# Optimization experiments

Hardware: AMD Instinct MI355X
Metric: run time of the kernel (lower is better)

Reference implementation:

```python
import jax, jax.numpy as jnp
import numpy as np

R = 32          # voxel resolution
EPS = 0.0       # normalization eps


def setup_inputs() -> dict:
    key = jax.random.key(0)
    k1, k2 = jax.random.split(key)
    B, D, N = 16, 64, 32768
    features = jax.random.normal(k1, (B, D, N), dtype=jnp.float32)
    coords = jax.random.normal(k2, (B, 3, N), dtype=jnp.float32)
    return {"features": features, "coords": coords}


def reference(features, coords):
    """features: (B, D, N), coords: (B, 3, N).
    Returns (voxel_features (B, D, R, R, R), norm_coords (B, 3, N))."""
    B, D, N = features.shape
    r = R

    # --- normalize coords into [0, r-1] (torch detaches coords; fwd math identical) ---
    nc = coords - coords.mean(axis=2, keepdims=True)                    # center
    norm = jnp.linalg.norm(nc, axis=1, keepdims=True)                   # (B,1,N)
    max_norm = norm.max(axis=2, keepdims=True)                          # (B,1,1)
    nc = nc / (max_norm * 2.0 + EPS) + 0.5
    norm_coords = jnp.clip(nc * r, 0, r - 1)                            # (B,3,N)
    vox = jnp.round(norm_coords).astype(jnp.int32)                      # (B,3,N)

    # --- scatter-mean features into r^3 voxels (avg_voxelize) ---
    idx = vox[:, 0] * (r * r) + vox[:, 1] * r + vox[:, 2]               # (B,N) in [0, r^3)
    flat_idx = (idx + jnp.arange(B, dtype=jnp.int32)[:, None] * (r ** 3)).reshape(-1)  # (B*N,)
    flat_feat = features.transpose(0, 2, 1).reshape(B * N, D)           # (B*N, D)

    sums = jax.ops.segment_sum(flat_feat, flat_idx, num_segments=B * r ** 3)   # (B*r^3, D)
    cnt = jax.ops.segment_sum(jnp.ones((B * N,), dtype=features.dtype),
                              flat_idx, num_segments=B * r ** 3)               # (B*r^3,)
    avg = sums / jnp.maximum(cnt, 1.0)[:, None]                          # empty voxels -> 0

    vox_feat = avg.reshape(B, r ** 3, D).transpose(0, 2, 1).reshape(B, D, r, r, r)
    return vox_feat, norm_coords
```

## Files before the change

kernel.cpp:

```cpp
#include <hip/hip_runtime.h>

#define RES 32
#define R3 (RES * RES * RES)

__global__ __launch_bounds__(1024) void stats_kernel(
        const float* __restrict__ coords,
        float* __restrict__ mean_out,
        float* __restrict__ denom_out,
        int* __restrict__ counts, int N) {
    const int b = blockIdx.x;
    const int tid = threadIdx.x;
    const float* cb = coords + (size_t)b * 3 * N;

    int4* cz = (int4*)(counts + (size_t)b * R3);
    const int4 zi = make_int4(0, 0, 0, 0);
    for (int i = tid; i < (R3 >> 2); i += 1024) cz[i] = zi;

    const int nvec = N >> 2;
    const float4* c0 = (const float4*)cb;
    const float4* c1 = (const float4*)(cb + N);
    const float4* c2 = (const float4*)(cb + 2 * N);
    float s0 = 0.f, s1 = 0.f, s2 = 0.f;
    for (int n = tid; n < nvec; n += 1024) {
        float4 a = c0[n]; s0 += (a.x + a.y) + (a.z + a.w);
        float4 c = c1[n]; s1 += (c.x + c.y) + (c.z + c.w);
        float4 d = c2[n]; s2 += (d.x + d.y) + (d.z + d.w);
    }
    if (tid == 0) {
        for (int n = nvec << 2; n < N; ++n) {
            s0 += cb[n]; s1 += cb[N + n]; s2 += cb[2 * N + n];
        }
    }
    for (int off = 32; off; off >>= 1) {
        s0 += __shfl_down(s0, off);
        s1 += __shfl_down(s1, off);
        s2 += __shfl_down(s2, off);
    }
    __shared__ float r0[16], r1[16], r2[16];
    __shared__ float mean_s[3];
    const int lane = tid & 63, wv = tid >> 6;
    if (lane == 0) { r0[wv] = s0; r1[wv] = s1; r2[wv] = s2; }
    __syncthreads();
    if (tid == 0) {
        float t0 = 0.f, t1 = 0.f, t2 = 0.f;
        for (int w = 0; w < 16; ++w) { t0 += r0[w]; t1 += r1[w]; t2 += r2[w]; }
        mean_s[0] = t0 / (float)N;
        mean_s[1] = t1 / (float)N;
        mean_s[2] = t2 / (float)N;
    }
    __syncthreads();
    const float m0 = mean_s[0], m1 = mean_s[1], m2 = mean_s[2];

    float mx = 0.f;
    for (int n = tid; n < nvec; n += 1024) {
        float4 a = c0[n], c = c1[n], d = c2[n];
        a.x -= m0; a.y -= m0; a.z -= m0; a.w -= m0;
        c.x -= m1; c.y -= m1; c.z -= m1; c.w -= m1;
        d.x -= m2; d.y -= m2; d.z -= m2; d.w -= m2;
        mx = fmaxf(mx, a.x * a.x + c.x * c.x + d.x * d.x);
        mx = fmaxf(mx, a.y * a.y + c.y * c.y + d.y * d.y);
        mx = fmaxf(mx, a.z * a.z + c.z * c.z + d.z * d.z);
        mx = fmaxf(mx, a.w * a.w + c.w * c.w + d.w * d.w);
    }
    if (tid == 0) {
        for (int n = nvec << 2; n < N; ++n) {
            float a = cb[n] - m0, c = cb[N + n] - m1, d = cb[2 * N + n] - m2;
            mx = fmaxf(mx, a * a + c * c + d * d);
        }
    }
    for (int off = 32; off; off >>= 1) mx = fmaxf(mx, __shfl_down(mx, off));
    if (lane == 0) r0[wv] = mx;
    __syncthreads();
    if (tid == 0) {
        for (int w = 0; w < 16; ++w) mx = fmaxf(mx, r0[w]);
        mean_out[b * 4 + 0] = m0;
        mean_out[b * 4 + 1] = m1;
        mean_out[b * 4 + 2] = m2;
        denom_out[b] = 2.0f * sqrtf(mx);
    }
}

__global__ void point_kernel(const float* __restrict__ coords,
                             const float* __restrict__ mean,
                             const float* __restrict__ denom_in,
                             float* __restrict__ nc_out,
                             unsigned short* __restrict__ idx_out,
                             int* __restrict__ counts, int N) {
    const int n4 = blockIdx.x * blockDim.x + threadIdx.x;
    const int b = blockIdx.y;
    const int nvec = (N + 3) >> 2;
    if (n4 >= nvec) return;

    const float* cb = coords + (size_t)b * 3 * N;
    const float m0 = mean[b * 4 + 0];
    const float m1 = mean[b * 4 + 1];
    const float m2 = mean[b * 4 + 2];
    const float denom = denom_in[b];
    float* ncb = nc_out + (size_t)b * 3 * N;
    unsigned short* irow = idx_out + (size_t)b * N;
    int* crow = counts + (size_t)b * R3;

    const int n0 = n4 << 2;
    if (n0 + 3 < N) {
        float4 a = *(const float4*)(cb + n0);
        float4 c = *(const float4*)(cb + N + n0);
        float4 d = *(const float4*)(cb + 2 * N + n0);
        float4 v0, v1, v2;
        int4 id;
        #define PROC(comp)                                                        \
        {                                                                         \
            float x = (a.comp - m0) / denom + 0.5f;                               \
            float y = (c.comp - m1) / denom + 0.5f;                               \
            float z = (d.comp - m2) / denom + 0.5f;                               \
            v0.comp = fminf(fmaxf(x * (float)RES, 0.f), (float)(RES - 1));        \
            v1.comp = fminf(fmaxf(y * (float)RES, 0.f), (float)(RES - 1));        \
            v2.comp = fminf(fmaxf(z * (float)RES, 0.f), (float)(RES - 1));        \
            id.comp = (int)rintf(v0.comp) * RES * RES                             \
                    + (int)rintf(v1.comp) * RES + (int)rintf(v2.comp);            \
        }
        PROC(x) PROC(y) PROC(z) PROC(w)
        #undef PROC
        *(float4*)(ncb + n0) = v0;
        *(float4*)(ncb + N + n0) = v1;
        *(float4*)(ncb + 2 * N + n0) = v2;
        ushort4 us;
        us.x = (unsigned short)id.x; us.y = (unsigned short)id.y;
        us.z = (unsigned short)id.z; us.w = (unsigned short)id.w;
        *(ushort4*)(irow + n0) = us;
        atomicAdd(&crow[id.x], 1);
        atomicAdd(&crow[id.y], 1);
        atomicAdd(&crow[id.z], 1);
        atomicAdd(&crow[id.w], 1);
    } else {
        for (int n = n0; n < N; ++n) {
            float x = (cb[n] - m0) / denom + 0.5f;
            float y = (cb[N + n] - m1) / denom + 0.5f;
            float z = (cb[2 * N + n] - m2) / denom + 0.5f;
            float v0 = fminf(fmaxf(x * (float)RES, 0.f), (float)(RES - 1));
            float v1 = fminf(fmaxf(y * (float)RES, 0.f), (float)(RES - 1));
            float v2 = fminf(fmaxf(z * (float)RES, 0.f), (float)(RES - 1));
            ncb[n] = v0; ncb[N + n] = v1; ncb[2 * N + n] = v2;
            int id = (int)rintf(v0) * RES * RES + (int)rintf(v1) * RES + (int)rintf(v2);
            irow[n] = (unsigned short)id;
            atomicAdd(&crow[id], 1);
        }
    }
}

__global__ __launch_bounds__(1024) void scanplist_kernel(
        const int* __restrict__ counts,
        const unsigned short* __restrict__ idx,
        unsigned short* __restrict__ start,
        unsigned short* __restrict__ plist, int N) {
    const int b = blockIdx.x;
    const int tid = threadIdx.x;
    const int lane = tid & 63, wv = tid >> 6;
    const int base = tid * 32;
    const int* crow = counts + (size_t)b * R3;

    __shared__ int cursor[R3];
    __shared__ int wsum[16], woff[16];

    int vals[32];
    int tot = 0;
    const int4* c4 = (const int4*)(crow + base);
    for (int i = 0; i < 8; ++i) {
        int4 t = c4[i];
        vals[4 * i + 0] = t.x; vals[4 * i + 1] = t.y;
        vals[4 * i + 2] = t.z; vals[4 * i + 3] = t.w;
        tot += (t.x + t.y) + (t.z + t.w);
    }
    int inc = tot;
    for (int o = 1; o < 64; o <<= 1) {
        int t = __shfl_up(inc, o);
        if (lane >= o) inc += t;
    }
    if (lane == 63) wsum[wv] = inc;
    __syncthreads();
    if (tid == 0) {
        int r = 0;
        for (int w = 0; w < 16; ++w) { woff[w] = r; r += wsum[w]; }
    }
    __syncthreads();
    int run = woff[wv] + inc - tot;
    unsigned short* srow = start + (size_t)b * R3 + base;
    for (int i = 0; i < 32; ++i) {
        srow[i] = (unsigned short)run;
        cursor[base + i] = run;
        run += vals[i];
    }
    __syncthreads();

    const unsigned short* irow = idx + (size_t)b * N;
    unsigned short* prow = plist + (size_t)b * N;
    for (int n = tid; n < N; n += 1024) {
        const int v = irow[n];
        const int pos = atomicAdd(&cursor[v], 1);
        prow[pos] = (unsigned short)n;
    }
}

__global__ __launch_bounds__(1024) void reduce_kernel(
        const float* __restrict__ feats,
        const unsigned short* __restrict__ plist,
        const unsigned short* __restrict__ start,
        const int* __restrict__ counts,
        float* __restrict__ vox, int D, int N) {
    const int d = blockIdx.x;
    const int b = blockIdx.y;
    const int tid = threadIdx.x;

    __shared__ float row[R3];
    const float* frow = feats + ((size_t)b * D + d) * N;
    {
        float4* r4 = (float4*)row;
        const float4* f4 = (const float4*)frow;
        for (int i = tid; i < (N >> 2); i += 1024) r4[i] = f4[i];
        if (tid == 0) for (int n = (N >> 2) << 2; n < N; ++n) row[n] = frow[n];
    }
    __syncthreads();

    const unsigned short* prow = plist + (size_t)b * N;
    const unsigned short* srow = start + (size_t)b * R3;
    const int* crow = counts + (size_t)b * R3;
    float* vrow = vox + ((size_t)b * D + d) * R3;

    for (int k = 0; k < R3 / 1024; ++k) {
        const int v = (k << 10) + tid;
        const int c = crow[v];
        const int s = srow[v];
        float a = 0.f;
        int j = 0;
        for (; j + 16 <= c; j += 16) {
            const unsigned short* pp = prow + s + j;
            const int p0 = pp[0],  p1 = pp[1],  p2 = pp[2],  p3 = pp[3];
            const int p4 = pp[4],  p5 = pp[5],  p6 = pp[6],  p7 = pp[7];
            const int p8 = pp[8],  p9 = pp[9],  pa = pp[10], pb = pp[11];
            const int pc = pp[12], pd = pp[13], pe = pp[14], pf = pp[15];
            float t0 = ((row[p0] + row[p1]) + (row[p2] + row[p3]))
                     + ((row[p4] + row[p5]) + (row[p6] + row[p7]));
            float t1 = ((row[p8] + row[p9]) + (row[pa] + row[pb]))
                     + ((row[pc] + row[pd]) + (row[pe] + row[pf]));
            a += t0 + t1;
        }
        for (; j + 4 <= c; j += 4) {
            const unsigned short* pp = prow + s + j;
            const int p0 = pp[0], p1 = pp[1], p2 = pp[2], p3 = pp[3];
            a += (row[p0] + row[p1]) + (row[p2] + row[p3]);
        }
        for (; j < c; ++j) a += row[prow[s + j]];
        vrow[v] = a / (float)(c > 1 ? c : 1);
    }
}

extern "C" void kernel_launch(void* const* d_in, const int* in_sizes, int n_in,
                              void* d_out, int out_size, void* d_ws, size_t ws_size,
                              hipStream_t stream) {
    const float* feats  = (const float*)d_in[0];
    const float* coords = (const float*)d_in[1];
    float* out = (float*)d_out;

    const int D = (int)(3LL * in_sizes[0] / in_sizes[1]);
    const int B = (int)((long long)(out_size - in_sizes[1]) / ((long long)D * R3));
    const int N = in_sizes[1] / (3 * B);

    float* vox_out = out;
    float* nc_out  = out + (size_t)B * D * R3;

    const size_t BR3 = (size_t)B * R3;
    const size_t BN  = (size_t)B * N;
    float*          mean   = (float*)d_ws;
    float*          denom  = (float*)((char*)d_ws + 1024);
    int*            counts = (int*)((char*)d_ws + 4096);
    unsigned short* start  = (unsigned short*)((char*)d_ws + 4096 + 4 * BR3);
    unsigned short* idx    = (unsigned short*)((char*)d_ws + 4096 + 6 * BR3);
    unsigned short* plist  = (unsigned short*)((char*)d_ws + 4096 + 6 * BR3 + 2 * BN);

    stats_kernel<<<dim3(B), dim3(1024), 0, stream>>>(coords, mean, denom, counts, N);

    const int nvec = (N + 3) >> 2;
    point_kernel<<<dim3((nvec + 255) / 256, B), dim3(256), 0, stream>>>(
        coords, mean, denom, nc_out, idx, counts, N);

    scanplist_kernel<<<dim3(B), dim3(1024), 0, stream>>>(counts, idx, start, plist, N);

    reduce_kernel<<<dim3(D, B), dim3(1024), 0, stream>>>(
        feats, plist, start, counts, vox_out, D, N);
}
```

Baseline: 458.2 us.

## Fuse all voxelization stages into one cooperative persistent kernel with sorted-key segmented reduction

```diff
diff --git a/kernel.cpp b/kernel.cpp
--- a/kernel.cpp
+++ b/kernel.cpp
@@ -1,255 +1,297 @@
 #include <hip/hip_runtime.h>
-
-#define RES 32
-#define R3 (RES * RES * RES)
-
-__global__ __launch_bounds__(1024) void stats_kernel(
-        const float* __restrict__ coords,
-        float* __restrict__ mean_out,
-        float* __restrict__ denom_out,
-        int* __restrict__ counts, int N) {
-    const int b = blockIdx.x;
+#include <hip/hip_cooperative_groups.h>
+namespace cg = cooperative_groups;
+
+#define RES  32
+#define R3   32768
+#define NBLK 256
+#define NTHR 1024
+
+struct Params {
+    const float* feats;
+    const float* coords;
+    float* vox;
+    float* nc;
+    float* accum;
+    unsigned* maxsq;
+    int* counts;
+    unsigned short* start;
+    int* cursor;
+    unsigned* keys;
+    unsigned* skeys;
+    int B, D, N;
+};
+
+__global__ __launch_bounds__(NTHR, 4) void fused_kernel(Params p) {
+    cg::grid_group grid = cg::this_grid();
     const int tid = threadIdx.x;
-    const float* cb = coords + (size_t)b * 3 * N;
-
-    int4* cz = (int4*)(counts + (size_t)b * R3);
-    const int4 zi = make_int4(0, 0, 0, 0);
-    for (int i = tid; i < (R3 >> 2); i += 1024) cz[i] = zi;
-
+    const int bid = blockIdx.x;
+    const int B = p.B, D = p.D, N = p.N;
+    const int lane = tid & 63, wv = tid >> 6;
+
+    __shared__ float row[R3];
+    __shared__ float red[3][16];
+    __shared__ unsigned short headv[NTHR];
+    __shared__ float headsum[NTHR];
+    __shared__ unsigned char contf[NTHR];
+    __shared__ int wsum[16], woff[16];
+
+    {
+        const int gtid = bid * NTHR + tid, gsz = NBLK * NTHR;
+        int4* c4 = (int4*)p.counts;
+        const int tot4 = (B * R3) >> 2;
+        for (int i = gtid; i < tot4; i += gsz) c4[i] = make_int4(0, 0, 0, 0);
+        if (bid == 0) {
+            if (tid < B * 4) p.accum[tid] = 0.f;
+            if (tid >= 256 && tid < 256 + B) p.maxsq[tid - 256] = 0u;
+        }
+    }
+    grid.sync();
+
+    const int b1 = bid % B;
+    const int chunk = bid / B;
+    const int pstride = (NBLK / B) * NTHR;
+    const float* cb = p.coords + (size_t)b1 * 3 * N;
     const int nvec = N >> 2;
     const float4* c0 = (const float4*)cb;
     const float4* c1 = (const float4*)(cb + N);
     const float4* c2 = (const float4*)(cb + 2 * N);
-    float s0 = 0.f, s1 = 0.f, s2 = 0.f;
-    for (int n = tid; n < nvec; n += 1024) {
-        float4 a = c0[n]; s0 += (a.x + a.y) + (a.z + a.w);
-        float4 c = c1[n]; s1 += (c.x + c.y) + (c.z + c.w);
-        float4 d = c2[n]; s2 += (d.x + d.y) + (d.z + d.w);
-    }
-    if (tid == 0) {
-        for (int n = nvec << 2; n < N; ++n) {
-            s0 += cb[n]; s1 += cb[N + n]; s2 += cb[2 * N + n];
-        }
-    }
-    for (int off = 32; off; off >>= 1) {
-        s0 += __shfl_down(s0, off);
-        s1 += __shfl_down(s1, off);
-        s2 += __shfl_down(s2, off);
-    }
-    __shared__ float r0[16], r1[16], r2[16];
-    __shared__ float mean_s[3];
-    const int lane = tid & 63, wv = tid >> 6;
-    if (lane == 0) { r0[wv] = s0; r1[wv] = s1; r2[wv] = s2; }
-    __syncthreads();
-    if (tid == 0) {
-        float t0 = 0.f, t1 = 0.f, t2 = 0.f;
-        for (int w = 0; w < 16; ++w) { t0 += r0[w]; t1 += r1[w]; t2 += r2[w]; }
-        mean_s[0] = t0 / (float)N;
-        mean_s[1] = t1 / (float)N;
-        mean_s[2] = t2 / (float)N;
-    }
-    __syncthreads();
-    const float m0 = mean_s[0], m1 = mean_s[1], m2 = mean_s[2];
-
-    float mx = 0.f;
-    for (int n = tid; n < nvec; n += 1024) {
-        float4 a = c0[n], c = c1[n], d = c2[n];
-        a.x -= m0; a.y -= m0; a.z -= m0; a.w -= m0;
-        c.x -= m1; c.y -= m1; c.z -= m1; c.w -= m1;
-        d.x -= m2; d.y -= m2; d.z -= m2; d.w -= m2;
-        mx = fmaxf(mx, a.x * a.x + c.x * c.x + d.x * d.x);
-        mx = fmaxf(mx, a.y * a.y + c.y * c.y + d.y * d.y);
-        mx = fmaxf(mx, a.z * a.z + c.z * c.z + d.z * d.z);
-        mx = fmaxf(mx, a.w * a.w + c.w * c.w + d.w * d.w);
-    }
-    if (tid == 0) {
-        for (int n = nvec << 2; n < N; ++n) {
-            float a = cb[n] - m0, c = cb[N + n] - m1, d = cb[2 * N + n] - m2;
-            mx = fmaxf(mx, a * a + c * c + d * d);
-        }
-    }
-    for (int off = 32; off; off >>= 1) mx = fmaxf(mx, __shfl_down(mx, off));
-    if (lane == 0) r0[wv] = mx;
-    __syncthreads();
-    if (tid == 0) {
-        for (int w = 0; w < 16; ++w) mx = fmaxf(mx, r0[w]);
-        mean_out[b * 4 + 0] = m0;
-        mean_out[b * 4 + 1] = m1;
-        mean_out[b * 4 + 2] = m2;
-        denom_out[b] = 2.0f * sqrtf(mx);
-    }
-}
-
-__global__ void point_kernel(const float* __restrict__ coords,
-                             const float* __restrict__ mean,
-                             const float* __restrict__ denom_in,
-                             float* __restrict__ nc_out,
-                             unsigned short* __restrict__ idx_out,
-                             int* __restrict__ counts, int N) {
-    const int n4 = blockIdx.x * blockDim.x + threadIdx.x;
-    const int b = blockIdx.y;
-    const int nvec = (N + 3) >> 2;
-    if (n4 >= nvec) return;
-
-    const float* cb = coords + (size_t)b * 3 * N;
-    const float m0 = mean[b * 4 + 0];
-    const float m1 = mean[b * 4 + 1];
-    const float m2 = mean[b * 4 + 2];
-    const float denom = denom_in[b];
-    float* ncb = nc_out + (size_t)b * 3 * N;
-    unsigned short* irow = idx_out + (size_t)b * N;
-    int* crow = counts + (size_t)b * R3;
-
-    const int n0 = n4 << 2;
-    if (n0 + 3 < N) {
-        float4 a = *(const float4*)(cb + n0);
-        float4 c = *(const float4*)(cb + N + n0);
-        float4 d = *(const float4*)(cb + 2 * N + n0);
-        float4 v0, v1, v2;
-        int4 id;
-        #define PROC(comp)                                                        \
-        {                                                                         \
-            float x = (a.comp - m0) / denom + 0.5f;                               \
-            float y = (c.comp - m1) / denom + 0.5f;                               \
-            float z = (d.comp - m2) / denom + 0.5f;                               \
-            v0.comp = fminf(fmaxf(x * (float)RES, 0.f), (float)(RES - 1));        \
-            v1.comp = fminf(fmaxf(y * (float)RES, 0.f), (float)(RES - 1));        \
-            v2.comp = fminf(fmaxf(z * (float)RES, 0.f), (float)(RES - 1));        \
-            id.comp = (int)rintf(v0.comp) * RES * RES                             \
-                    + (int)rintf(v1.comp) * RES + (int)rintf(v2.comp);            \
-        }
-        PROC(x) PROC(y) PROC(z) PROC(w)
-        #undef PROC
-        *(float4*)(ncb + n0) = v0;
-        *(float4*)(ncb + N + n0) = v1;
-        *(float4*)(ncb + 2 * N + n0) = v2;
-        ushort4 us;
-        us.x = (unsigned short)id.x; us.y = (unsigned short)id.y;
-        us.z = (unsigned short)id.z; us.w = (unsigned short)id.w;
-        *(ushort4*)(irow + n0) = us;
-        atomicAdd(&crow[id.x], 1);
-        atomicAdd(&crow[id.y], 1);
-        atomicAdd(&crow[id.z], 1);
-        atomicAdd(&crow[id.w], 1);
-    } else {
-        for (int n = n0; n < N; ++n) {
-            float x = (cb[n] - m0) / denom + 0.5f;
-            float y = (cb[N + n] - m1) / denom + 0.5f;
-            float z = (cb[2 * N + n] - m2) / denom + 0.5f;
-            float v0 = fminf(fmaxf(x * (float)RES, 0.f), (float)(RES - 1));
-            float v1 = fminf(fmaxf(y * (float)RES, 0.f), (float)(RES - 1));
-            float v2 = fminf(fmaxf(z * (float)RES, 0.f), (float)(RES - 1));
-            ncb[n] = v0; ncb[N + n] = v1; ncb[2 * N + n] = v2;
-            int id = (int)rintf(v0) * RES * RES + (int)rintf(v1) * RES + (int)rintf(v2);
-            irow[n] = (unsigned short)id;
-            atomicAdd(&crow[id], 1);
-        }
-    }
-}
-
-__global__ __launch_bounds__(1024) void scanplist_kernel(
-        const int* __restrict__ counts,
-        const unsigned short* __restrict__ idx,
-        unsigned short* __restrict__ start,
-        unsigned short* __restrict__ plist, int N) {
-    const int b = blockIdx.x;
-    const int tid = threadIdx.x;
-    const int lane = tid & 63, wv = tid >> 6;
-    const int base = tid * 32;
-    const int* crow = counts + (size_t)b * R3;
-
-    __shared__ int cursor[R3];
-    __shared__ int wsum[16], woff[16];
-
-    int vals[32];
-    int tot = 0;
-    const int4* c4 = (const int4*)(crow + base);
-    for (int i = 0; i < 8; ++i) {
-        int4 t = c4[i];
-        vals[4 * i + 0] = t.x; vals[4 * i + 1] = t.y;
-        vals[4 * i + 2] = t.z; vals[4 * i + 3] = t.w;
-        tot += (t.x + t.y) + (t.z + t.w);
-    }
-    int inc = tot;
-    for (int o = 1; o < 64; o <<= 1) {
-        int t = __shfl_up(inc, o);
-        if (lane >= o) inc += t;
-    }
-    if (lane == 63) wsum[wv] = inc;
-    __syncthreads();
-    if (tid == 0) {
-        int r = 0;
-        for (int w = 0; w < 16; ++w) { woff[w] = r; r += wsum[w]; }
-    }
-    __syncthreads();
-    int run = woff[wv] + inc - tot;
-    unsigned short* srow = start + (size_t)b * R3 + base;
-    for (int i = 0; i < 32; ++i) {
-        srow[i] = (unsigned short)run;
-        cursor[base + i] = run;
-        run += vals[i];
-    }
-    __syncthreads();
-
-    const unsigned short* irow = idx + (size_t)b * N;
-    unsigned short* prow = plist + (size_t)b * N;
-    for (int n = tid; n < N; n += 1024) {
-        const int v = irow[n];
-        const int pos = atomicAdd(&cursor[v], 1);
-        prow[pos] = (unsigned short)n;
-    }
-}
-
-__global__ __launch_bounds__(1024) void reduce_kernel(
-        const float* __restrict__ feats,
-        const unsigned short* __restrict__ plist,
-        const unsigned short* __restrict__ start,
-        const int* __restrict__ counts,
-        float* __restrict__ vox, int D, int N) {
-    const int d = blockIdx.x;
-    const int b = blockIdx.y;
-    const int tid = threadIdx.x;
-
-    __shared__ float row[R3];
-    const float* frow = feats + ((size_t)b * D + d) * N;
-    {
-        float4* r4 = (float4*)row;
-        const float4* f4 = (const float4*)frow;
-        for (int i = tid; i < (N >> 2); i += 1024) r4[i] = f4[i];
-        if (tid == 0) for (int n = (N >> 2) << 2; n < N; ++n) row[n] = frow[n];
-    }
-    __syncthreads();
-
-    const unsigned short* prow = plist + (size_t)b * N;
-    const unsigned short* srow = start + (size_t)b * R3;
-    const int* crow = counts + (size_t)b * R3;
-    float* vrow = vox + ((size_t)b * D + d) * R3;
-
-    for (int k = 0; k < R3 / 1024; ++k) {
-        const int v = (k << 10) + tid;
-        const int c = crow[v];
-        const int s = srow[v];
-        float a = 0.f;
-        int j = 0;
-        for (; j + 16 <= c; j += 16) {
-            const unsigned short* pp = prow + s + j;
-            const int p0 = pp[0],  p1 = pp[1],  p2 = pp[2],  p3 = pp[3];
-            const int p4 = pp[4],  p5 = pp[5],  p6 = pp[6],  p7 = pp[7];
-            const int p8 = pp[8],  p9 = pp[9],  pa = pp[10], pb = pp[11];
-            const int pc = pp[12], pd = pp[13], pe = pp[14], pf = pp[15];
-            float t0 = ((row[p0] + row[p1]) + (row[p2] + row[p3]))
-                     + ((row[p4] + row[p5]) + (row[p6] + row[p7]));
-            float t1 = ((row[p8] + row[p9]) + (row[pa] + row[pb]))
-                     + ((row[pc] + row[pd]) + (row[pe] + row[pf]));
-            a += t0 + t1;
-        }
-        for (; j + 4 <= c; j += 4) {
-            const unsigned short* pp = prow + s + j;
-            const int p0 = pp[0], p1 = pp[1], p2 = pp[2], p3 = pp[3];
-            a += (row[p0] + row[p1]) + (row[p2] + row[p3]);
-        }
-        for (; j < c; ++j) a += row[prow[s + j]];
-        vrow[v] = a / (float)(c > 1 ? c : 1);
+
+    {
+        float s0 = 0.f, s1 = 0.f, s2 = 0.f;
+        for (int n = chunk * NTHR + tid; n < nvec; n += pstride) {
+            float4 a = c0[n]; s0 += (a.x + a.y) + (a.z + a.w);
+            float4 c = c1[n]; s1 += (c.x + c.y) + (c.z + c.w);
+            float4 d = c2[n]; s2 += (d.x + d.y) + (d.z + d.w);
+        }
+        if (chunk == 0 && tid == 0)
+            for (int n = nvec << 2; n < N; ++n) { s0 += cb[n]; s1 += cb[N + n]; s2 += cb[2 * N + n]; }
+        for (int o = 32; o; o >>= 1) {
+            s0 += __shfl_down(s0, o); s1 += __shfl_down(s1, o); s2 += __shfl_down(s2, o);
+        }
+        if (lane == 0) { red[0][wv] = s0; red[1][wv] = s1; red[2][wv] = s2; }
+        __syncthreads();
+        if (tid == 0) {
+            float t0 = 0.f, t1 = 0.f, t2 = 0.f;
+            for (int w = 0; w < 16; ++w) { t0 += red[0][w]; t1 += red[1][w]; t2 += red[2][w]; }
+            unsafeAtomicAdd(&p.accum[b1 * 4 + 0], t0);
+            unsafeAtomicAdd(&p.accum[b1 * 4 + 1], t1);
+            unsafeAtomicAdd(&p.accum[b1 * 4 + 2], t2);
+        }
+        __syncthreads();
+    }
+    grid.sync();
+
+    const float m0 = p.accum[b1 * 4 + 0] / (float)N;
+    const float m1 = p.accum[b1 * 4 + 1] / (float)N;
+    const float m2 = p.accum[b1 * 4 + 2] / (float)N;
+
+    {
+        float mx = 0.f;
+        for (int n = chunk * NTHR + tid; n < nvec; n += pstride) {
+            float4 a = c0[n], c = c1[n], d = c2[n];
+            a.x -= m0; a.y -= m0; a.z -= m0; a.w -= m0;
+            c.x -= m1; c.y -= m1; c.z -= m1; c.w -= m1;
+            d.x -= m2; d.y -= m2; d.z -= m2; d.w -= m2;
+            mx = fmaxf(mx, a.x * a.x + c.x * c.x + d.x * d.x);
+            mx = fmaxf(mx, a.y * a.y + c.y * c.y + d.y * d.y);
+            mx = fmaxf(mx, a.z * a.z + c.z * c.z + d.z * d.z);
+            mx = fmaxf(mx, a.w * a.w + c.w * c.w + d.w * d.w);
+        }
+        if (chunk == 0 && tid == 0)
+            for (int n = nvec << 2; n < N; ++n) {
+                float a = cb[n] - m0, c = cb[N + n] - m1, d = cb[2 * N + n] - m2;
+                mx = fmaxf(mx, a * a + c * c + d * d);
+            }
+        for (int o = 32; o; o >>= 1) mx = fmaxf(mx, __shfl_down(mx, o));
+        if (lane == 0) red[0][wv] = mx;
+        __syncthreads();
+        if (tid == 0) {
+            for (int w = 0; w < 16; ++w) mx = fmaxf(mx, red[0][w]);
+            atomicMax(&p.maxsq[b1], __float_as_uint(mx));
+        }
+        __syncthreads();
+    }
+    grid.sync();
+
+    {
+        const float denom = 2.0f * sqrtf(__uint_as_float(p.maxsq[b1]));
+        float* ncb = p.nc + (size_t)b1 * 3 * N;
+        unsigned* krow = p.keys + (size_t)b1 * N;
+        int* crow = p.counts + (size_t)b1 * R3;
+        for (int n4 = chunk * NTHR + tid; n4 < nvec; n4 += pstride) {
+            const int n0 = n4 << 2;
+            float4 a = c0[n4], c = c1[n4], d = c2[n4];
+            float4 v0, v1, v2; int4 id;
+            #define PROC(comp)                                                    \
+            {                                                                     \
+                float x = (a.comp - m0) / denom + 0.5f;                           \
+                float y = (c.comp - m1) / denom + 0.5f;                           \
+                float z = (d.comp - m2) / denom + 0.5f;                           \
+                v0.comp = fminf(fmaxf(x * (float)RES, 0.f), (float)(RES - 1));    \
+                v1.comp = fminf(fmaxf(y * (float)RES, 0.f), (float)(RES - 1));    \
+                v2.comp = fminf(fmaxf(z * (float)RES, 0.f), (float)(RES - 1));    \
+                id.comp = (int)rintf(v0.comp) * RES * RES                         \
+                        + (int)rintf(v1.comp) * RES + (int)rintf(v2.comp);        \
+            }
+            PROC(x) PROC(y) PROC(z) PROC(w)
+            #undef PROC
+            *(float4*)(ncb + n0) = v0;
+            *(float4*)(ncb + N + n0) = v1;
+            *(float4*)(ncb + 2 * N + n0) = v2;
+            uint4 k;
+            k.x = ((unsigned)id.x << 16) | (unsigned)(n0 + 0);
+            k.y = ((unsigned)id.y << 16) | (unsigned)(n0 + 1);
+            k.z = ((unsigned)id.z << 16) | (unsigned)(n0 + 2);
+            k.w = ((unsigned)id.w << 16) | (unsigned)(n0 + 3);
+            *(uint4*)(krow + n0) = k;
+            atomicAdd(&crow[id.x], 1);
+            atomicAdd(&crow[id.y], 1);
+            atomicAdd(&crow[id.z], 1);
+            atomicAdd(&crow[id.w], 1);
+        }
+        if (chunk == 0 && tid == 0) {
+            for (int n = nvec << 2; n < N; ++n) {
+                float x = (cb[n] - m0) / denom + 0.5f;
+                float y = (cb[N + n] - m1) / denom + 0.5f;
+                float z = (cb[2 * N + n] - m2) / denom + 0.5f;
+                float v0 = fminf(fmaxf(x * (float)RES, 0.f), (float)(RES - 1));
+                float v1 = fminf(fmaxf(y * (float)RES, 0.f), (float)(RES - 1));
+                float v2 = fminf(fmaxf(z * (float)RES, 0.f), (float)(RES - 1));
+                ncb[n] = v0; ncb[N + n] = v1; ncb[2 * N + n] = v2;
+                int id = (int)rintf(v0) * RES * RES + (int)rintf(v1) * RES + (int)rintf(v2);
+                krow[n] = ((unsigned)id << 16) | (unsigned)n;
+                atomicAdd(&crow[id], 1);
+            }
+        }
+    }
+    grid.sync();
+
+    if (bid < B) {
+        const int* crow = p.counts + (size_t)bid * R3;
+        int vals[32]; int tot = 0;
+        const int4* c4 = (const int4*)(crow + tid * 32);
+        for (int i = 0; i < 8; ++i) {
+            int4 t = c4[i];
+            vals[4 * i + 0] = t.x; vals[4 * i + 1] = t.y;
+            vals[4 * i + 2] = t.z; vals[4 * i + 3] = t.w;
+            tot += (t.x + t.y) + (t.z + t.w);
+        }
+        int inc = tot;
+        for (int o = 1; o < 64; o <<= 1) {
+            int t = __shfl_up(inc, o);
+            if (lane >= o) inc += t;
+        }
+        if (lane == 63) wsum[wv] = inc;
+        __syncthreads();
+        if (tid == 0) { int r = 0; for (int w = 0; w < 16; ++w) { woff[w] = r; r += wsum[w]; } }
+        __syncthreads();
+        int run = woff[wv] + inc - tot;
+        unsigned short* srow = p.start + (size_t)bid * R3 + tid * 32;
+        int* urow = p.cursor + (size_t)bid * R3 + tid * 32;
+        for (int i = 0; i < 32; ++i) {
+            srow[i] = (unsigned short)run;
+            urow[i] = run;
+            run += vals[i];
+        }
+    }
+    grid.sync();
+
+    {
+        const unsigned* krow = p.keys + (size_t)b1 * N;
+        unsigned* skrow = p.skeys + (size_t)b1 * N;
+        int* curs = p.cursor + (size_t)b1 * R3;
+        for (int n = chunk * NTHR + tid; n < N; n += pstride) {
+            unsigned key = krow[n];
+            int pos = atomicAdd(&curs[key >> 16], 1);
+            skrow[pos] = key;
+        }
+    }
+    grid.sync();
+
+    const int tiles = B * D;
+    const int PPT = (N + NTHR - 1) / NTHR;
+    for (int tile = bid; tile < tiles; tile += NBLK) {
+        const int b = tile / D, d = tile % D;
+        __syncthreads();
+        {
+            const float* frow = p.feats + ((size_t)b * D + d) * N;
+            float4* r4 = (float4*)row;
+            const float4* f4 = (const float4*)frow;
+            for (int i = tid; i < (N >> 2); i += NTHR) r4[i] = f4[i];
+            if (tid == 0) for (int n = (N >> 2) << 2; n < N; ++n) row[n] = frow[n];
+        }
+        __syncthreads();
+
+        const unsigned* skrow = p.skeys + (size_t)b * N;
+        const unsigned short* srow = p.start + (size_t)b * R3;
+        const int* crow = p.counts + (size_t)b * R3;
+        float* vrow = p.vox + ((size_t)b * D + d) * R3;
+
+        const int p0 = tid * PPT;
+        const int pend = min(p0 + PPT, N);
+
+        unsigned cur = 0xFFFFFFFFu;
+        float sum = 0.f;
+        int seg_start = p0;
+        unsigned short hv = 0xFFFFu; float hs = 0.f; unsigned char cont = 0;
+
+        auto step = [&](unsigned key, int gpos) {
+            unsigned v = key >> 16;
+            float val = row[key & 0xFFFFu];
+            if (cur == 0xFFFFFFFFu) { cur = v; sum = val; seg_start = gpos; }
+            else if (v == cur) { sum += val; }
+            else {
+                if ((int)srow[cur] == seg_start) {
+                    int c = crow[cur];
+                    vrow[cur] = sum / (float)(c > 1 ? c : 1);
+                } else { hv = (unsigned short)cur; hs = sum; }
+                cur = v; sum = val; seg_start = gpos;
+            }
+        };
+
+        if (p0 < N) {
+            int g = p0;
+            if (((PPT & 7) == 0) && pend == p0 + PPT) {
+                for (; g < pend; g += 8) {
+                    uint4 k0 = *(const uint4*)(skrow + g);
+                    uint4 k1 = *(const uint4*)(skrow + g + 4);
+                    step(k0.x, g + 0); step(k0.y, g + 1);
+                    step(k0.z, g + 2); step(k0.w, g + 3);
+                    step(k1.x, g + 4); step(k1.y, g + 5);
+                    step(k1.z, g + 6); step(k1.w, g + 7);
+                }
+            } else {
+                for (; g < pend; ++g) step(skrow[g], g);
+            }
+        }
+
+        bool tail_owned = false;
+        unsigned tv = 0; float ts = 0.f;
+        if (p0 < N) {
+            if ((int)srow[cur] == seg_start) { tail_owned = true; tv = cur; ts = sum; }
+            else { hv = (unsigned short)cur; hs = sum; cont = 1; }
+        }
+        headv[tid] = hv; headsum[tid] = hs; contf[tid] = cont;
+        __syncthreads();
+        if (tail_owned) {
+            float total = ts;
+            for (int u = tid + 1; u < NTHR; ++u) {
+                if (headv[u] != (unsigned short)tv) break;
+                total += headsum[u];
+                if (!contf[u]) break;
+            }
+            int c = crow[tv];
+            vrow[tv] = total / (float)(c > 1 ? c : 1);
+        }
+        for (int i = tid; i < (R3 >> 2); i += NTHR) {
+            int4 c = ((const int4*)crow)[i];
+            const int v0 = i << 2;
+            if (c.x == 0) vrow[v0 + 0] = 0.f;
+            if (c.y == 0) vrow[v0 + 1] = 0.f;
+            if (c.z == 0) vrow[v0 + 2] = 0.f;
+            if (c.w == 0) vrow[v0 + 3] = 0.f;
+        }
     }
 }
 
@@ -264,26 +306,23 @@
     const int B = (int)((long long)(out_size - in_sizes[1]) / ((long long)D * R3));
     const int N = in_sizes[1] / (3 * B);
 
-    float* vox_out = out;
-    float* nc_out  = out + (size_t)B * D * R3;
-
     const size_t BR3 = (size_t)B * R3;
     const size_t BN  = (size_t)B * N;
-    float*          mean   = (float*)d_ws;
-    float*          denom  = (float*)((char*)d_ws + 1024);
-    int*            counts = (int*)((char*)d_ws + 4096);
-    unsigned short* start  = (unsigned short*)((char*)d_ws + 4096 + 4 * BR3);
-    unsigned short* idx    = (unsigned short*)((char*)d_ws + 4096 + 6 * BR3);
-    unsigned short* plist  = (unsigned short*)((char*)d_ws + 4096 + 6 * BR3 + 2 * BN);
-
-    stats_kernel<<<dim3(B), dim3(1024), 0, stream>>>(coords, mean, denom, counts, N);
-
-    const int nvec = (N + 3) >> 2;
-    point_kernel<<<dim3((nvec + 255) / 256, B), dim3(256), 0, stream>>>(
-        coords, mean, denom, nc_out, idx, counts, N);
-
-    scanplist_kernel<<<dim3(B), dim3(1024), 0, stream>>>(counts, idx, start, plist, N);
-
-    reduce_kernel<<<dim3(D, B), dim3(1024), 0, stream>>>(
-        feats, plist, start, counts, vox_out, D, N);
+
+    Params prm;
+    prm.feats  = feats;
+    prm.coords = coords;
+    prm.vox    = out;
+    prm.nc     = out + (size_t)B * D * R3;
+    prm.accum  = (float*)d_ws;
+    prm.maxsq  = (unsigned*)((char*)d_ws + 1024);
+    prm.counts = (int*)((char*)d_ws + 4096);
+    prm.start  = (unsigned short*)((char*)d_ws + 4096 + 4 * BR3);
+    prm.cursor = (int*)((char*)d_ws + 4096 + 6 * BR3);
+    prm.keys   = (unsigned*)((char*)d_ws + 4096 + 10 * BR3);
+    prm.skeys  = (unsigned*)((char*)d_ws + 4096 + 10 * BR3 + 4 * BN);
+    prm.B = B; prm.D = D; prm.N = N;
+
+    void* args[] = { &prm };
+    hipLaunchCooperativeKernel(fused_kernel, dim3(NBLK), dim3(NTHR), args, 0, stream);
 }
```

After: 596.1 us. 1.3x slower.
